# Kernel optimization log

Measured on AMD Instinct MI355X. Metric: run time of the kernel, lower is better.

The kernel has to match this reference:

```python
import jax, jax.numpy as jnp
import numpy as np

NUM_BINS = 32


def setup_inputs() -> dict:
    key = jax.random.key(0)
    k1, k2, k3 = jax.random.split(key, 3)
    shape = (16, 3, 512, 512)  # NCHW images in [0,1)
    pred = jax.random.uniform(k1, shape, dtype=jnp.float32)
    target = jax.random.uniform(k2, shape, dtype=jnp.float32)
    input_img = jax.random.uniform(k3, shape, dtype=jnp.float32)
    return {"pred": pred, "target": target, "input_img": input_img}


def _binned_means(values, seg_ids, num_segments):
    # per-(channel,bin) masked mean; empty bins -> 0.0 (matches torch branch)
    sums = jax.ops.segment_sum(values, seg_ids, num_segments=num_segments)
    counts = jax.ops.segment_sum(jnp.ones_like(values), seg_ids, num_segments=num_segments)
    return jnp.where(counts > 0, sums / jnp.maximum(counts, 1.0), 0.0)


def reference(pred, target, input_img):
    nb = NUM_BINS
    edges = jnp.linspace(0.0, 1.0, nb + 1)

    # [3, N] per-channel flattened views (channel-major)
    x = jnp.transpose(input_img, (1, 0, 2, 3)).reshape(3, -1)
    p = jnp.transpose(pred, (1, 0, 2, 3)).reshape(-1)
    t = jnp.transpose(target, (1, 0, 2, 3)).reshape(-1)

    # bin i covers [edges[i], edges[i+1]) -> searchsorted(side='right') - 1
    idx = jnp.searchsorted(edges, x, side="right") - 1  # [3, N]
    valid = (idx >= 0) & (idx < nb)  # x == 1.0 or x < 0 falls in no bin
    # fold channel into segment id; invalid ids are out-of-range and dropped
    seg = jnp.where(valid, idx + jnp.arange(3)[:, None] * nb, 3 * nb).reshape(-1)

    pred_curve = _binned_means(p, seg, 3 * nb)    # [3*nb]
    target_curve = _binned_means(t, seg, 3 * nb)  # [3*nb]

    # sum_c l1(pred_curve_c, target_curve_c) / 3 == mean over all 3*nb entries
    return jnp.mean(jnp.abs(pred_curve - target_curve))
```

## Files before the change

### kernel.cpp

```cpp
#include <hip/hip_runtime.h>

#define NB     32
#define NSEG   96
#define TPB    256
#define NROW   128
#define PAD    33
#define F4PT   8
#define NCOPY  32

#define POISON8 0xAAAAAAAAAAAAAAAAull
#define POISON4 0xAAAAAAAAu

typedef float f4 __attribute__((ext_vector_type(4)));

union SMem {
    unsigned int hist[NROW * PAD];
    double       red[128];
};

__global__ __launch_bounds__(TPB, 4) void ccl_fused(
    const f4* __restrict__ pred,
    const f4* __restrict__ target,
    const f4* __restrict__ img,
    long n4,
    unsigned long long* __restrict__ gdiff,
    unsigned int* __restrict__ gcnt,
    unsigned int* __restrict__ done,
    float* __restrict__ out)
{
    __shared__ SMem sm;
    __shared__ int lastflag;

    const int tid = threadIdx.x;
    for (int i = tid; i < NROW * PAD; i += TPB) sm.hist[i] = 0u;
    __syncthreads();

    const long base = (long)blockIdx.x * (TPB * F4PT);
    const int  c    = (int)((base >> 16) % 3);
    unsigned int* h = &sm.hist[(tid >> 1) * PAD];

    f4 xv[F4PT], pv[F4PT], tv[F4PT];
    const bool full = (base + (long)TPB * F4PT) <= n4;

    if (full) {
#pragma unroll
        for (int q = 0; q < F4PT; ++q) {
            long i = base + (long)q * TPB + tid;
            xv[q] = __builtin_nontemporal_load(&img[i]);
            pv[q] = __builtin_nontemporal_load(&pred[i]);
            tv[q] = __builtin_nontemporal_load(&target[i]);
        }
        __builtin_amdgcn_sched_barrier(0);
#pragma unroll
        for (int q = 0; q < F4PT; ++q) {
            float xs[4] = {xv[q].x, xv[q].y, xv[q].z, xv[q].w};
            float ps[4] = {pv[q].x, pv[q].y, pv[q].z, pv[q].w};
            float ts[4] = {tv[q].x, tv[q].y, tv[q].z, tv[q].w};
#pragma unroll
            for (int e = 0; e < 4; ++e) {
                float xe = xs[e];
                if (xe >= 0.0f && xe < 1.0f) {
                    int b = (int)(xe * 32.0f);
                    float d = ps[e] - ts[e];
                    unsigned pack = (unsigned)fmaf(d, 65536.0f, 131072.5f) + (1u << 24);
                    atomicAdd(&h[b], pack);
                }
            }
        }
    } else {
#pragma unroll
        for (int q = 0; q < F4PT; ++q) {
            long i = base + (long)q * TPB + tid;
            if (i >= n4) continue;
            f4 xq = __builtin_nontemporal_load(&img[i]);
            f4 pq = __builtin_nontemporal_load(&pred[i]);
            f4 tq = __builtin_nontemporal_load(&target[i]);
            float xs[4] = {xq.x, xq.y, xq.z, xq.w};
            float ps[4] = {pq.x, pq.y, pq.z, pq.w};
            float ts[4] = {tq.x, tq.y, tq.z, tq.w};
#pragma unroll
            for (int e = 0; e < 4; ++e) {
                float xe = xs[e];
                if (xe >= 0.0f && xe < 1.0f) {
                    int b = (int)(xe * 32.0f);
                    float d = ps[e] - ts[e];
                    unsigned pack = (unsigned)fmaf(d, 65536.0f, 131072.5f) + (1u << 24);
                    atomicAdd(&h[b], pack);
                }
            }
        }
    }
    __syncthreads();

    unsigned fx = 0u, cn = 0u;
    {
        int b = tid & 31, g = tid >> 5;
#pragma unroll
        for (int k = 0; k < 16; ++k) {
            unsigned v = sm.hist[(g * 16 + k) * PAD + b];
            cn += v >> 24;
            fx += v & 0xFFFFFFu;
        }
    }
    __syncthreads();
    sm.hist[tid]       = fx;
    sm.hist[TPB + tid] = cn;
    __syncthreads();

    if (tid < 32) {
        unsigned fxt = 0u, cnt = 0u;
#pragma unroll
        for (int k = 0; k < 8; ++k) {
            fxt += sm.hist[tid + 32 * k];
            cnt += sm.hist[TPB + tid + 32 * k];
        }
        if (cnt > 0u) {
            int s = (int)(fxt - (cnt << 17));
            int cp = (int)(blockIdx.x & (NCOPY - 1));
            atomicAdd(&gdiff[cp * NSEG + c * NB + tid], (unsigned long long)(long long)s);
            atomicAdd(&gcnt [cp * NSEG + c * NB + tid], cnt);
        }
    }

    asm volatile("s_waitcnt vmcnt(0)" ::: "memory");
    __syncthreads();
    if (tid == 0) {
        unsigned old = __hip_atomic_fetch_add(done, 1u, __ATOMIC_RELAXED,
                                              __HIP_MEMORY_SCOPE_AGENT);
        lastflag = (old == POISON4 + (unsigned)gridDim.x - 1u);
    }
    __syncthreads();
    if (!lastflag) return;

    double v = 0.0;
    if (tid < NSEG) {
        unsigned long long ds = 0ull;
        unsigned int       ct = 0u;
#pragma unroll
        for (int k = 0; k < NCOPY; ++k) {
            ds += __hip_atomic_load(&gdiff[k * NSEG + tid], __ATOMIC_RELAXED, __HIP_MEMORY_SCOPE_AGENT);
            ct += __hip_atomic_load(&gcnt [k * NSEG + tid], __ATOMIC_RELAXED, __HIP_MEMORY_SCOPE_AGENT);
        }
        ds -= (unsigned long long)NCOPY * POISON8;
        ct -= (unsigned)NCOPY * POISON4;
        if (ct > 0u) {
            double dt = (double)(long long)ds * (1.0 / 65536.0);
            v = fabs(dt / (double)ct);
        }
    }
    if (tid < 128) sm.red[tid] = v;
    __syncthreads();
    for (int off = 64; off > 0; off >>= 1) {
        if (tid < off) sm.red[tid] += sm.red[tid + off];
        __syncthreads();
    }
    if (tid == 0) out[0] = (float)(sm.red[0] / (double)NSEG);
}

extern "C" void kernel_launch(void* const* d_in, const int* in_sizes, int n_in,
                              void* d_out, int out_size, void* d_ws, size_t ws_size,
                              hipStream_t stream) {
    const f4* pred   = (const f4*)d_in[0];
    const f4* target = (const f4*)d_in[1];
    const f4* img    = (const f4*)d_in[2];
    long n4 = (long)in_sizes[0] / 4;

    unsigned long long* gdiff = (unsigned long long*)d_ws;
    unsigned int*       gcnt  = (unsigned int*)((char*)d_ws + (size_t)NCOPY * NSEG * sizeof(unsigned long long));
    unsigned int*       done  = (unsigned int*)((char*)d_ws + (size_t)NCOPY * NSEG * (sizeof(unsigned long long) + sizeof(unsigned int)));


    int nblocks = (int)((n4 + (long)TPB * F4PT - 1) / ((long)TPB * F4PT));
    ccl_fused<<<dim3(nblocks), dim3(TPB), 0, stream>>>(pred, target, img, n4,
                                                       gdiff, gcnt, done, (float*)d_out);
}
```

Baseline: 155.5 us.

## Give each thread a private LDS histogram row and pipeline loads with staged waitcnt

Doubles the histogram rows so each thread owns its own row, removing LDS atomic contention between thread pairs and letting each thread zero its own row without a block barrier. Replaces the compiler nontemporal loads with inline-asm global loads and consumes each quad after a partial vmcnt wait, overlapping histogram work with outstanding memory traffic. This costs twice the LDS footprint and twice the reduction reads, which may limit occupancy.

Result: no change. 157.5 us (+1.3%).

```diff
diff --git a/kernel.cpp b/kernel.cpp
--- a/kernel.cpp
+++ b/kernel.cpp
@@ -3,7 +3,7 @@
 #define NB     32
 #define NSEG   96
 #define TPB    256
-#define NROW   128
+#define NROW   256
 #define PAD    33
 #define F4PT   8
 #define NCOPY  32
@@ -13,10 +13,36 @@
 
 typedef float f4 __attribute__((ext_vector_type(4)));
 
-union SMem {
+union __align__(16) SMem {
     unsigned int hist[NROW * PAD];
     double       red[128];
 };
+
+#define NTLOAD(dst, voff, base) \
+    asm volatile("global_load_dwordx4 %0, %1, %2 nt" \
+                 : "=v"(dst) : "v"(voff), "s"(base))
+
+#define WAITQ(N) \
+    do { asm volatile("s_waitcnt vmcnt(" #N ")" ::: "memory"); \
+         __builtin_amdgcn_sched_barrier(0); } while (0)
+
+#define CONSUME(q) do { \
+    float xs[4] = {xv[q].x, xv[q].y, xv[q].z, xv[q].w}; \
+    float ps[4] = {pv[q].x, pv[q].y, pv[q].z, pv[q].w}; \
+    float ts[4] = {tv[q].x, tv[q].y, tv[q].z, tv[q].w}; \
+    _Pragma("unroll") \
+    for (int e = 0; e < 4; ++e) { \
+        float xe = xs[e]; \
+         \
+        if (xe >= 0.0f && xe < 1.0f) { \
+            int b = (int)(xe * 32.0f); \
+            float d = ps[e] - ts[e];                  \
+             \
+            unsigned pack = (unsigned)fmaf(d, 65536.0f, 131072.5f) + (1u << 24); \
+            atomicAdd(&h[b], pack);                   \
+        } \
+    } \
+} while (0)
 
 __global__ __launch_bounds__(TPB, 4) void ccl_fused(
     const f4* __restrict__ pred,
@@ -32,45 +58,40 @@
     __shared__ int lastflag;
 
     const int tid = threadIdx.x;
-    for (int i = tid; i < NROW * PAD; i += TPB) sm.hist[i] = 0u;
-    __syncthreads();
-
-    const long base = (long)blockIdx.x * (TPB * F4PT);
-    const int  c    = (int)((base >> 16) % 3);
-    unsigned int* h = &sm.hist[(tid >> 1) * PAD];
+    const long base0 = (long)blockIdx.x * (TPB * F4PT);
+    const int  c = (int)((base0 >> 16) % 3);
+    unsigned int* h = &sm.hist[tid * PAD];
 
     f4 xv[F4PT], pv[F4PT], tv[F4PT];
-    const bool full = (base + (long)TPB * F4PT) <= n4;
+    const bool full = (base0 + (long)TPB * F4PT) <= n4;
 
     if (full) {
+        unsigned vo[F4PT];
+#pragma unroll
+        for (int q = 0; q < F4PT; ++q)
+            vo[q] = (unsigned)((base0 + (long)q * TPB + tid) * 16);
 #pragma unroll
         for (int q = 0; q < F4PT; ++q) {
-            long i = base + (long)q * TPB + tid;
-            xv[q] = __builtin_nontemporal_load(&img[i]);
-            pv[q] = __builtin_nontemporal_load(&pred[i]);
-            tv[q] = __builtin_nontemporal_load(&target[i]);
+            NTLOAD(xv[q], vo[q], img);
+            NTLOAD(pv[q], vo[q], pred);
+            NTLOAD(tv[q], vo[q], target);
         }
-        __builtin_amdgcn_sched_barrier(0);
+#pragma unroll
+        for (int k = 0; k < NB; ++k) h[k] = 0u;
+        WAITQ(21); CONSUME(0);
+        WAITQ(18); CONSUME(1);
+        WAITQ(15); CONSUME(2);
+        WAITQ(12); CONSUME(3);
+        WAITQ(9);  CONSUME(4);
+        WAITQ(6);  CONSUME(5);
+        WAITQ(3);  CONSUME(6);
+        WAITQ(0);  CONSUME(7);
+    } else {
+#pragma unroll
+        for (int k = 0; k < NB; ++k) h[k] = 0u;
 #pragma unroll
         for (int q = 0; q < F4PT; ++q) {
-            float xs[4] = {xv[q].x, xv[q].y, xv[q].z, xv[q].w};
-            float ps[4] = {pv[q].x, pv[q].y, pv[q].z, pv[q].w};
-            float ts[4] = {tv[q].x, tv[q].y, tv[q].z, tv[q].w};
-#pragma unroll
-            for (int e = 0; e < 4; ++e) {
-                float xe = xs[e];
-                if (xe >= 0.0f && xe < 1.0f) {
-                    int b = (int)(xe * 32.0f);
-                    float d = ps[e] - ts[e];
-                    unsigned pack = (unsigned)fmaf(d, 65536.0f, 131072.5f) + (1u << 24);
-                    atomicAdd(&h[b], pack);
-                }
-            }
-        }
-    } else {
-#pragma unroll
-        for (int q = 0; q < F4PT; ++q) {
-            long i = base + (long)q * TPB + tid;
+            long i = base0 + (long)q * TPB + tid;
             if (i >= n4) continue;
             f4 xq = __builtin_nontemporal_load(&img[i]);
             f4 pq = __builtin_nontemporal_load(&pred[i]);
@@ -96,8 +117,8 @@
     {
         int b = tid & 31, g = tid >> 5;
 #pragma unroll
-        for (int k = 0; k < 16; ++k) {
-            unsigned v = sm.hist[(g * 16 + k) * PAD + b];
+        for (int k = 0; k < 32; ++k) {
+            unsigned v = sm.hist[(g * 32 + k) * PAD + b];
             cn += v >> 24;
             fx += v & 0xFFFFFFu;
         }
```
